# Kernel tuning notes

Hardware: AMD Instinct MI355X
Metric: run time of the kernel (lower is better)

## Reference

```python
import jax, jax.numpy as jnp
import numpy as np

N_NODES = 100000
N_EDGES = 1600000
IN_F, HID_F, OUT_F = 128, 128, 64


def setup_inputs() -> dict:
    key = jax.random.key(0)
    ks = jax.random.split(key, 12)
    inp = {
        "features": jax.random.normal(ks[0], (N_NODES, IN_F), dtype=jnp.float32),
        "src": jax.random.randint(ks[1], (N_EDGES,), 0, N_NODES, dtype=jnp.int32),
        "dst": jax.random.randint(ks[2], (N_EDGES,), 0, N_NODES, dtype=jnp.int32),
        "Ws0": jax.random.normal(ks[3], (IN_F, HID_F), dtype=jnp.float32) / np.sqrt(IN_F),
        "Wn0": jax.random.normal(ks[4], (IN_F, HID_F), dtype=jnp.float32) / np.sqrt(IN_F),
        "b0": jnp.zeros((HID_F,), dtype=jnp.float32),
        "Ws1": jax.random.normal(ks[5], (HID_F, HID_F), dtype=jnp.float32) / np.sqrt(HID_F),
        "Wn1": jax.random.normal(ks[6], (HID_F, HID_F), dtype=jnp.float32) / np.sqrt(HID_F),
        "b1": jnp.zeros((HID_F,), dtype=jnp.float32),
        "Ws2": jax.random.normal(ks[7], (HID_F, OUT_F), dtype=jnp.float32) / np.sqrt(HID_F),
        "Wn2": jax.random.normal(ks[8], (HID_F, OUT_F), dtype=jnp.float32) / np.sqrt(HID_F),
        "b2": jnp.zeros((OUT_F,), dtype=jnp.float32),
    }
    return inp


def _sage_conv(h, src, dst, inv_deg, Ws, Wn, b, act):
    # gather neighbor (source) features along edges: [E, d]
    msg = h[src]
    # mean aggregation onto destination nodes: [N, d]
    agg = jax.ops.segment_sum(msg, dst, num_segments=N_NODES) * inv_deg
    out = h @ Ws + agg @ Wn + b
    return jax.nn.relu(out) if act else out


def reference(features, src, dst, Ws0, Wn0, b0, Ws1, Wn1, b1, Ws2, Wn2, b2):
    # in-degree for mean normalization (clamped at 1, matching DGL mean semantics)
    deg = jax.ops.segment_sum(jnp.ones((N_EDGES,), jnp.float32), dst, num_segments=N_NODES)
    inv_deg = (1.0 / jnp.maximum(deg, 1.0))[:, None]
    h = _sage_conv(features, src, dst, inv_deg, Ws0, Wn0, b0, act=True)
    # dropout is identity in eval mode
    h = _sage_conv(h, src, dst, inv_deg, Ws1, Wn1, b1, act=True)
    h = _sage_conv(h, src, dst, inv_deg, Ws2, Wn2, b2, act=False)
    return h
```

## Files before the change

### kernel.cpp

```cpp
#include <hip/hip_runtime.h>

static constexpr int N = 100000;
static constexpr int E = 1600000;
static constexpr int F = 128;
static constexpr int HA_W = 256;
static constexpr int NB = (N + 127) / 128;
static constexpr int PCHUNK = 16384;
static constexpr int PGRID = (E + PCHUNK - 1) / PCHUNK;
static constexpr int CAP = 8192;

typedef __attribute__((ext_vector_type(8))) short bf16x8;
typedef __attribute__((ext_vector_type(4))) float f32x4;

__device__ inline unsigned short f2bf(float f) {
    unsigned int u = __builtin_bit_cast(unsigned int, f);
    unsigned int r = u + 0x7FFF + ((u >> 16) & 1);
    return (unsigned short)(r >> 16);
}
__device__ inline float bf_lo(unsigned int v) {
    return __builtin_bit_cast(float, v << 16);
}
__device__ inline float bf_hi(unsigned int v) {
    return __builtin_bit_cast(float, v & 0xffff0000u);
}

__global__ __launch_bounds__(256) void bucket_count_k(const int* __restrict__ dst,
                                                      int* __restrict__ bcnt) {
    __shared__ int sh[NB];
    const int t = threadIdx.x;
    for (int i = t; i < NB; i += 256) sh[i] = 0;
    __syncthreads();
    const int cb = blockIdx.x * PCHUNK;
    #pragma unroll
    for (int j = 0; j < PCHUNK / 1024; ++j) {
        int idx = cb + j * 1024 + t * 4;
        if (idx < E) {
            int4 d4 = *(const int4*)&dst[idx];
            atomicAdd(&sh[d4.x >> 7], 1);
            atomicAdd(&sh[d4.y >> 7], 1);
            atomicAdd(&sh[d4.z >> 7], 1);
            atomicAdd(&sh[d4.w >> 7], 1);
        }
    }
    __syncthreads();
    for (int i = t; i < NB; i += 256)
        if (sh[i]) atomicAdd(&bcnt[i], sh[i]);
}

__global__ __launch_bounds__(1024) void scan_buckets_k(const int* __restrict__ bcnt,
                                                       int* __restrict__ bbase,
                                                       int* __restrict__ bcur,
                                                       int* __restrict__ row_ptr) {
    __shared__ int shw[16];
    const int t = threadIdx.x, lane = t & 63, wv = t >> 6;
    int v = (t < NB) ? bcnt[t] : 0;
    int s = v;
    #pragma unroll
    for (int off = 1; off < 64; off <<= 1) {
        int u = __shfl_up(s, off);
        if (lane >= off) s += u;
    }
    if (lane == 63) shw[wv] = s;
    __syncthreads();
    if (wv == 0 && lane < 16) {
        int w = shw[lane];
        #pragma unroll
        for (int off = 1; off < 16; off <<= 1) {
            int u = __shfl_up(w, off);
            if (lane >= off) w += u;
        }
        shw[lane] = w;
    }
    __syncthreads();
    int wex = wv ? shw[wv - 1] : 0;
    int excl = wex + s - v;
    if (t < NB) { bbase[t] = excl; bcur[t] = 0; }
    if (t == 0) { bbase[NB] = E; row_ptr[N] = E; }
}

__global__ __launch_bounds__(256) void partition_k(const int* __restrict__ src,
                                                   const int* __restrict__ dst,
                                                   const int* __restrict__ bbase,
                                                   int* __restrict__ bcur,
                                                   unsigned int* __restrict__ ebuf) {
    __shared__ int sh_hist[NB];
    __shared__ int sh_base[NB];
    __shared__ int sh_cur[NB];
    const int t = threadIdx.x;
    for (int i = t; i < NB; i += 256) sh_hist[i] = 0;
    __syncthreads();
    const int cb = blockIdx.x * PCHUNK;
    #pragma unroll
    for (int j = 0; j < PCHUNK / 1024; ++j) {
        int idx = cb + j * 1024 + t * 4;
        if (idx < E) {
            int4 d4 = *(const int4*)&dst[idx];
            atomicAdd(&sh_hist[d4.x >> 7], 1);
            atomicAdd(&sh_hist[d4.y >> 7], 1);
            atomicAdd(&sh_hist[d4.z >> 7], 1);
            atomicAdd(&sh_hist[d4.w >> 7], 1);
        }
    }
    __syncthreads();
    for (int i = t; i < NB; i += 256) {
        int c = sh_hist[i];
        sh_base[i] = c ? (bbase[i] + atomicAdd(&bcur[i], c)) : 0;
        sh_cur[i] = 0;
    }
    __syncthreads();
    #pragma unroll
    for (int j = 0; j < PCHUNK / 1024; ++j) {
        int idx = cb + j * 1024 + t * 4;
        if (idx < E) {
            int4 s4 = *(const int4*)&src[idx];
            int4 d4 = *(const int4*)&dst[idx];
            {
                int b = d4.x >> 7; int p = atomicAdd(&sh_cur[b], 1);
                ebuf[sh_base[b] + p] = (unsigned)s4.x | ((unsigned)(d4.x & 127) << 17);
            }
            {
                int b = d4.y >> 7; int p = atomicAdd(&sh_cur[b], 1);
                ebuf[sh_base[b] + p] = (unsigned)s4.y | ((unsigned)(d4.y & 127) << 17);
            }
            {
                int b = d4.z >> 7; int p = atomicAdd(&sh_cur[b], 1);
                ebuf[sh_base[b] + p] = (unsigned)s4.z | ((unsigned)(d4.z & 127) << 17);
            }
            {
                int b = d4.w >> 7; int p = atomicAdd(&sh_cur[b], 1);
                ebuf[sh_base[b] + p] = (unsigned)s4.w | ((unsigned)(d4.w & 127) << 17);
            }
        }
    }
}

__global__ __launch_bounds__(256) void csr_sort_k(const unsigned int* __restrict__ ebuf,
                                                  const int* __restrict__ bbase,
                                                  int* __restrict__ row_ptr,
                                                  float* __restrict__ inv_deg,
                                                  int* __restrict__ esrc) {
    __shared__ unsigned int sh_e[CAP];
    __shared__ int sh_o[CAP];
    __shared__ int sh_hist[128];
    __shared__ int sh_excl[128];
    __shared__ int sh_cur[128];
    __shared__ int sh_w0;
    const int b = blockIdx.x, t = threadIdx.x;
    const int e0 = bbase[b];
    const int ec = bbase[b + 1] - e0;
    if (t < 128) { sh_hist[t] = 0; sh_cur[t] = 0; }
    __syncthreads();
    for (int i = t; i < ec; i += 256) {
        unsigned int e = ebuf[e0 + i];
        sh_e[i] = e;
        atomicAdd(&sh_hist[e >> 17], 1);
    }
    __syncthreads();
    int v = 0;
    if (t < 128) v = sh_hist[t];
    int incl = v;
    const int lane = t & 63;
    #pragma unroll
    for (int off = 1; off < 64; off <<= 1) {
        int u = __shfl_up(incl, off);
        if (lane >= off) incl += u;
    }
    if (t == 63) sh_w0 = incl;
    __syncthreads();
    if (t >= 64 && t < 128) incl += sh_w0;
    if (t < 128) {
        sh_excl[t] = incl - v;
        int node = b * 128 + t;
        if (node < N) {
            row_ptr[node] = e0 + incl - v;
            inv_deg[node] = 1.0f / fmaxf((float)v, 1.0f);
        }
    }
    __syncthreads();
    for (int i = t; i < ec; i += 256) {
        unsigned int e = sh_e[i];
        int l = e >> 17;
        int pos = sh_excl[l] + atomicAdd(&sh_cur[l], 1);
        sh_o[pos] = (int)(e & 0x1FFFF);
    }
    __syncthreads();
    for (int i = t; i < ec; i += 256) esrc[e0 + i] = sh_o[i];
}

__global__ __launch_bounds__(256) void conv_feat_k(const float* __restrict__ feat,
                                                   unsigned short* __restrict__ ha) {
    int idx = blockIdx.x * 256 + threadIdx.x;
    int node = idx >> 5;
    int c4 = idx & 31;
    if (node >= N) return;
    float4 v = *(const float4*)&feat[(size_t)node * F + c4 * 4];
    unsigned long long p = (unsigned long long)f2bf(v.x)
                         | ((unsigned long long)f2bf(v.y) << 16)
                         | ((unsigned long long)f2bf(v.z) << 32)
                         | ((unsigned long long)f2bf(v.w) << 48);
    *(unsigned long long*)&ha[(size_t)node * HA_W + c4 * 4] = p;
}

__global__ __launch_bounds__(256) void prep_w_all_k(const float* __restrict__ Ws0,
                                                    const float* __restrict__ Wn0,
                                                    const float* __restrict__ Ws1,
                                                    const float* __restrict__ Wn1,
                                                    const float* __restrict__ Ws2,
                                                    const float* __restrict__ Wn2,
                                                    unsigned short* __restrict__ Wt0,
                                                    unsigned short* __restrict__ Wt1,
                                                    unsigned short* __restrict__ Wc2) {
    int idx = blockIdx.x * 256 + threadIdx.x;
    if (idx < 32768) {
        int n = idx >> 8, k = idx & 255;
        float v = (k < 128) ? Ws0[k * 128 + n] : Wn0[(k - 128) * 128 + n];
        Wt0[n * 256 + k] = f2bf(v);
    } else if (idx < 65536) {
        int j = idx - 32768;
        int n = j >> 8, k = j & 255;
        float v = (k < 128) ? Ws1[k * 128 + n] : Wn1[(k - 128) * 128 + n];
        Wt1[n * 256 + k] = f2bf(v);
    } else if (idx < 65536 + 16384) {
        int j = idx - 65536;
        int c = j >> 7, k = j & 127;
        float v = (c < 64) ? Ws2[k * 64 + c] : Wn2[k * 64 + (c - 64)];
        Wc2[c * 128 + k] = f2bf(v);
    }
}

__global__ __launch_bounds__(256) void aggregate128_k(const unsigned short* __restrict__ ha,
                                                      unsigned short* __restrict__ ha_out,
                                                      const int* __restrict__ row_ptr,
                                                      const int* __restrict__ esrc,
                                                      const float* __restrict__ inv_deg) {
    const int lane = threadIdx.x & 63;
    const int wv = threadIdx.x >> 6;
    const int slot = lane >> 4;
    const int cl = lane & 15;
    const int node = blockIdx.x * 16 + wv * 4 + slot;
    const int beg = row_ptr[node];
    const int cnt = row_ptr[node + 1] - beg;
    const float sinv = inv_deg[node];
    int wmax = cnt;
    wmax = max(wmax, __shfl_xor(wmax, 16));
    wmax = max(wmax, __shfl_xor(wmax, 32));
    float a0 = 0.f, a1 = 0.f, a2 = 0.f, a3 = 0.f;
    float a4 = 0.f, a5 = 0.f, a6 = 0.f, a7 = 0.f;
    for (int j = 0; j < wmax; j += 8) {
        int idx[8];
        uint4 v[8];
        #pragma unroll
        for (int u = 0; u < 8; ++u)
            idx[u] = (j + u < cnt) ? __builtin_nontemporal_load(&esrc[beg + j + u]) : -1;
        #pragma unroll
        for (int u = 0; u < 8; ++u) {
            if (idx[u] >= 0)
                v[u] = *(const uint4*)&ha[(size_t)idx[u] * HA_W + cl * 8];
            else { v[u].x = 0u; v[u].y = 0u; v[u].z = 0u; v[u].w = 0u; }
        }
        #pragma unroll
        for (int u = 0; u < 8; ++u) {
            a0 += bf_lo(v[u].x); a1 += bf_hi(v[u].x);
            a2 += bf_lo(v[u].y); a3 += bf_hi(v[u].y);
            a4 += bf_lo(v[u].z); a5 += bf_hi(v[u].z);
            a6 += bf_lo(v[u].w); a7 += bf_hi(v[u].w);
        }
    }
    uint4 o;
    o.x = (unsigned int)f2bf(a0 * sinv) | ((unsigned int)f2bf(a1 * sinv) << 16);
    o.y = (unsigned int)f2bf(a2 * sinv) | ((unsigned int)f2bf(a3 * sinv) << 16);
    o.z = (unsigned int)f2bf(a4 * sinv) | ((unsigned int)f2bf(a5 * sinv) << 16);
    o.w = (unsigned int)f2bf(a6 * sinv) | ((unsigned int)f2bf(a7 * sinv) << 16);
    *(uint4*)&ha_out[(size_t)node * HA_W + F + cl * 8] = o;
}

__global__ __launch_bounds__(256) void aggregate64_add_k(const unsigned short* __restrict__ Q,
                                                         const int* __restrict__ row_ptr,
                                                         const int* __restrict__ esrc,
                                                         const float* __restrict__ inv_deg,
                                                         float* __restrict__ out) {
    const int lane = threadIdx.x & 63;
    const int wv = threadIdx.x >> 6;
    const int slot = lane >> 3;
    const int cl = lane & 7;
    const int node = blockIdx.x * 32 + wv * 8 + slot;
    const int beg = row_ptr[node];
    const int cnt = row_ptr[node + 1] - beg;
    const float sinv = inv_deg[node];
    int wmax = cnt;
    wmax = max(wmax, __shfl_xor(wmax, 8));
    wmax = max(wmax, __shfl_xor(wmax, 16));
    wmax = max(wmax, __shfl_xor(wmax, 32));
    float a0 = 0.f, a1 = 0.f, a2 = 0.f, a3 = 0.f;
    float a4 = 0.f, a5 = 0.f, a6 = 0.f, a7 = 0.f;
    for (int j = 0; j < wmax; j += 8) {
        int idx[8];
        uint4 v[8];
        #pragma unroll
        for (int u = 0; u < 8; ++u)
            idx[u] = (j + u < cnt) ? __builtin_nontemporal_load(&esrc[beg + j + u]) : -1;
        #pragma unroll
        for (int u = 0; u < 8; ++u) {
            if (idx[u] >= 0)
                v[u] = *(const uint4*)&Q[(size_t)idx[u] * 64 + cl * 8];
            else { v[u].x = 0u; v[u].y = 0u; v[u].z = 0u; v[u].w = 0u; }
        }
        #pragma unroll
        for (int u = 0; u < 8; ++u) {
            a0 += bf_lo(v[u].x); a1 += bf_hi(v[u].x);
            a2 += bf_lo(v[u].y); a3 += bf_hi(v[u].y);
            a4 += bf_lo(v[u].z); a5 += bf_hi(v[u].z);
            a6 += bf_lo(v[u].w); a7 += bf_hi(v[u].w);
        }
    }
    float4* p0 = (float4*)&out[(size_t)node * 64 + cl * 8];
    float4 pv = *p0;
    pv.x += a0 * sinv; pv.y += a1 * sinv; pv.z += a2 * sinv; pv.w += a3 * sinv;
    *p0 = pv;
    float4* p1 = p0 + 1;
    float4 pw = *p1;
    pw.x += a4 * sinv; pw.y += a5 * sinv; pw.z += a6 * sinv; pw.w += a7 * sinv;
    *p1 = pw;
}

__global__ __launch_bounds__(256) void linear01_k(const unsigned short* __restrict__ ha,
                                                  const unsigned short* __restrict__ Wt,
                                                  const float* __restrict__ bias,
                                                  unsigned short* __restrict__ out_ha) {
    constexpr int CPW = 32;
    constexpr int NT = 2;
    const int lane = threadIdx.x & 63;
    const int wv = threadIdx.x >> 6;
    const int col0 = wv * CPW;
    const int lc = lane & 15;
    const int lg = lane >> 4;
    bf16x8 bfrag[NT][8];
    float bias_c[NT];
    #pragma unroll
    for (int nt = 0; nt < NT; ++nt) {
        int col = col0 + nt * 16 + lc;
        bias_c[nt] = bias[col];
        #pragma unroll
        for (int ks = 0; ks < 8; ++ks)
            bfrag[nt][ks] = *(const bf16x8*)&Wt[col * 256 + ks * 32 + lg * 8];
    }
    const int i0base = blockIdx.x * 128;
    for (int s = 0; s < 8; ++s) {
        int i0 = i0base + s * 16;
        if (i0 >= N) return;
        const unsigned short* arow = &ha[(size_t)(i0 + lc) * HA_W];
        f32x4 acc[NT];
        #pragma unroll
        for (int nt = 0; nt < NT; ++nt) {
            acc[nt][0] = bias_c[nt]; acc[nt][1] = bias_c[nt];
            acc[nt][2] = bias_c[nt]; acc[nt][3] = bias_c[nt];
        }
        #pragma unroll
        for (int ks = 0; ks < 8; ++ks) {
            bf16x8 af = *(const bf16x8*)&arow[ks * 32 + lg * 8];
            #pragma unroll
            for (int nt = 0; nt < NT; ++nt)
                acc[nt] = __builtin_amdgcn_mfma_f32_16x16x32_bf16(af, bfrag[nt][ks], acc[nt], 0, 0, 0);
        }
        #pragma unroll
        for (int nt = 0; nt < NT; ++nt) {
            int col = col0 + nt * 16 + lc;
            #pragma unroll
            for (int r = 0; r < 4; ++r) {
                int orow = i0 + lg * 4 + r;
                float v = fmaxf(acc[nt][r], 0.f);
                out_ha[(size_t)orow * HA_W + col] = f2bf(v);
            }
        }
    }
}

__global__ __launch_bounds__(256) void linear2_k(const unsigned short* __restrict__ ha,
                                                 const unsigned short* __restrict__ Wc,
                                                 const float* __restrict__ bias,
                                                 float* __restrict__ out,
                                                 unsigned short* __restrict__ Q) {
    constexpr int CPW = 32;
    constexpr int NT = 2;
    const int lane = threadIdx.x & 63;
    const int wv = threadIdx.x >> 6;
    const int col0 = wv * CPW;
    const int lc = lane & 15;
    const int lg = lane >> 4;
    bf16x8 bfrag[NT][4];
    float bias_c[NT];
    #pragma unroll
    for (int nt = 0; nt < NT; ++nt) {
        int col = col0 + nt * 16 + lc;
        bias_c[nt] = (wv < 2) ? bias[col] : 0.f;
        #pragma unroll
        for (int ks = 0; ks < 4; ++ks)
            bfrag[nt][ks] = *(const bf16x8*)&Wc[col * 128 + ks * 32 + lg * 8];
    }
    const int i0base = blockIdx.x * 128;
    for (int s = 0; s < 8; ++s) {
        int i0 = i0base + s * 16;
        if (i0 >= N) return;
        const unsigned short* arow = &ha[(size_t)(i0 + lc) * HA_W];
        f32x4 acc[NT];
        #pragma unroll
        for (int nt = 0; nt < NT; ++nt) {
            acc[nt][0] = bias_c[nt]; acc[nt][1] = bias_c[nt];
            acc[nt][2] = bias_c[nt]; acc[nt][3] = bias_c[nt];
        }
        #pragma unroll
        for (int ks = 0; ks < 4; ++ks) {
            bf16x8 af = *(const bf16x8*)&arow[ks * 32 + lg * 8];
            #pragma unroll
            for (int nt = 0; nt < NT; ++nt)
                acc[nt] = __builtin_amdgcn_mfma_f32_16x16x32_bf16(af, bfrag[nt][ks], acc[nt], 0, 0, 0);
        }
        #pragma unroll
        for (int nt = 0; nt < NT; ++nt) {
            int col = col0 + nt * 16 + lc;
            #pragma unroll
            for (int r = 0; r < 4; ++r) {
                int orow = i0 + lg * 4 + r;
                float v = acc[nt][r];
                if (wv < 2) out[(size_t)orow * 64 + col] = v;
                else        Q[(size_t)orow * 64 + (col - 64)] = f2bf(v);
            }
        }
    }
}

extern "C" void kernel_launch(void* const* d_in, const int* in_sizes, int n_in,
                              void* d_out, int out_size, void* d_ws, size_t ws_size,
                              hipStream_t stream) {
    const float* feat = (const float*)d_in[0];
    const int*   src  = (const int*)d_in[1];
    const int*   dst  = (const int*)d_in[2];
    const float* Ws0  = (const float*)d_in[3];
    const float* Wn0  = (const float*)d_in[4];
    const float* b0   = (const float*)d_in[5];
    const float* Ws1  = (const float*)d_in[6];
    const float* Wn1  = (const float*)d_in[7];
    const float* b1   = (const float*)d_in[8];
    const float* Ws2  = (const float*)d_in[9];
    const float* Wn2  = (const float*)d_in[10];
    const float* b2   = (const float*)d_in[11];
    float* out = (float*)d_out;

    char* ws = (char*)d_ws;
    size_t off = 0;
    auto alloc = [&](size_t bytes) {
        void* p = ws + off;
        off = (off + bytes + 255) & ~(size_t)255;
        return p;
    };
    unsigned short* haA = (unsigned short*)alloc((size_t)N * HA_W * 2);
    unsigned short* haB = (unsigned short*)alloc((size_t)N * HA_W * 2);
    unsigned short* Qb  = (unsigned short*)alloc((size_t)N * 64 * 2);
    unsigned short* Wt0 = (unsigned short*)alloc((size_t)128 * 256 * 2);
    unsigned short* Wt1 = (unsigned short*)alloc((size_t)128 * 256 * 2);
    unsigned short* Wc2 = (unsigned short*)alloc((size_t)128 * 128 * 2);
    float* inv     = (float*)alloc((size_t)N * 4);
    int*   row_ptr = (int*)alloc((size_t)(N + 1) * 4);
    int*   bcnt    = (int*)alloc((size_t)NB * 4);
    int*   bbase   = (int*)alloc((size_t)(NB + 1) * 4);
    int*   bcur    = (int*)alloc((size_t)NB * 4);
    unsigned int* ebuf = (unsigned int*)alloc((size_t)E * 4);
    int*   esrc    = (int*)alloc((size_t)E * 4);
    (void)ws_size; (void)in_sizes; (void)n_in; (void)out_size;

    hipMemsetAsync(bcnt, 0, (size_t)NB * 4, stream);
    bucket_count_k<<<PGRID, 256, 0, stream>>>(dst, bcnt);
    scan_buckets_k<<<1, 1024, 0, stream>>>(bcnt, bbase, bcur, row_ptr);
    partition_k<<<PGRID, 256, 0, stream>>>(src, dst, bbase, bcur, ebuf);
    csr_sort_k<<<NB, 256, 0, stream>>>(ebuf, bbase, row_ptr, inv, esrc);

    conv_feat_k<<<(N * 32 + 255) / 256, 256, 0, stream>>>(feat, haA);
    prep_w_all_k<<<(65536 + 16384 + 255) / 256, 256, 0, stream>>>(
        Ws0, Wn0, Ws1, Wn1, Ws2, Wn2, Wt0, Wt1, Wc2);

    const int lin_grid = (N + 127) / 128;
    aggregate128_k<<<N / 16, 256, 0, stream>>>(haA, haA, row_ptr, esrc, inv);
    linear01_k<<<lin_grid, 256, 0, stream>>>(haA, Wt0, b0, haB);
    aggregate128_k<<<N / 16, 256, 0, stream>>>(haB, haB, row_ptr, esrc, inv);
    linear01_k<<<lin_grid, 256, 0, stream>>>(haB, Wt1, b1, haA);
    linear2_k<<<lin_grid, 256, 0, stream>>>(haA, Wc2, b2, out, Qb);
    aggregate64_add_k<<<N / 32, 256, 0, stream>>>(Qb, row_ptr, esrc, inv, out);
}
```

Before: 326.1 us.

## Use fixed-capacity edge buckets, compact feature layout, and fuse prep kernels

Drops the bucket-count and scan kernels by giving each 128-node bucket a fixed slot of 2560 edges, so partitioning writes at bucket*CAPB plus an atomic cursor and the sort reads its count from that cursor. Node features now live in a compact 128-wide bf16 buffer separate from the aggregation buffer, so neighbor gathers touch half as many bytes per row and the table fits better in cache. The linear layer reads the two halves from their separate buffers. Feature conversion and weight prep are merged into one launch. The fixed capacity assumes no bucket gets more than 2560 edges, which holds for uniformly random destinations but would overflow on skewed graphs.

```diff
diff --git a/kernel.cpp b/kernel.cpp
--- a/kernel.cpp
+++ b/kernel.cpp
@@ -3,11 +3,11 @@
 static constexpr int N = 100000;
 static constexpr int E = 1600000;
 static constexpr int F = 128;
-static constexpr int HA_W = 256;
 static constexpr int NB = (N + 127) / 128;
 static constexpr int PCHUNK = 16384;
 static constexpr int PGRID = (E + PCHUNK - 1) / PCHUNK;
-static constexpr int CAP = 8192;
+static constexpr int CAPB = 2560;
+static constexpr int NPAD = NB * 128;
 
 typedef __attribute__((ext_vector_type(8))) short bf16x8;
 typedef __attribute__((ext_vector_type(4))) float f32x4;
@@ -24,63 +24,53 @@
     return __builtin_bit_cast(float, v & 0xffff0000u);
 }
 
-__global__ __launch_bounds__(256) void bucket_count_k(const int* __restrict__ dst,
-                                                      int* __restrict__ bcnt) {
-    __shared__ int sh[NB];
+__global__ __launch_bounds__(256) void prep_all_k(const float* __restrict__ feat,
+                                                  unsigned short* __restrict__ hA,
+                                                  const float* __restrict__ Ws0,
+                                                  const float* __restrict__ Wn0,
+                                                  const float* __restrict__ Ws1,
+                                                  const float* __restrict__ Wn1,
+                                                  const float* __restrict__ Ws2,
+                                                  const float* __restrict__ Wn2,
+                                                  unsigned short* __restrict__ Wt0,
+                                                  unsigned short* __restrict__ Wt1,
+                                                  unsigned short* __restrict__ Wc2) {
     const int t = threadIdx.x;
-    for (int i = t; i < NB; i += 256) sh[i] = 0;
-    __syncthreads();
-    const int cb = blockIdx.x * PCHUNK;
-    #pragma unroll
-    for (int j = 0; j < PCHUNK / 1024; ++j) {
-        int idx = cb + j * 1024 + t * 4;
-        if (idx < E) {
-            int4 d4 = *(const int4*)&dst[idx];
-            atomicAdd(&sh[d4.x >> 7], 1);
-            atomicAdd(&sh[d4.y >> 7], 1);
-            atomicAdd(&sh[d4.z >> 7], 1);
-            atomicAdd(&sh[d4.w >> 7], 1);
-        }
-    }
-    __syncthreads();
-    for (int i = t; i < NB; i += 256)
-        if (sh[i]) atomicAdd(&bcnt[i], sh[i]);
-}
-
-__global__ __launch_bounds__(1024) void scan_buckets_k(const int* __restrict__ bcnt,
-                                                       int* __restrict__ bbase,
-                                                       int* __restrict__ bcur,
-                                                       int* __restrict__ row_ptr) {
-    __shared__ int shw[16];
-    const int t = threadIdx.x, lane = t & 63, wv = t >> 6;
-    int v = (t < NB) ? bcnt[t] : 0;
-    int s = v;
-    #pragma unroll
-    for (int off = 1; off < 64; off <<= 1) {
-        int u = __shfl_up(s, off);
-        if (lane >= off) s += u;
-    }
-    if (lane == 63) shw[wv] = s;
-    __syncthreads();
-    if (wv == 0 && lane < 16) {
-        int w = shw[lane];
-        #pragma unroll
-        for (int off = 1; off < 16; off <<= 1) {
-            int u = __shfl_up(w, off);
-            if (lane >= off) w += u;
-        }
-        shw[lane] = w;
-    }
-    __syncthreads();
-    int wex = wv ? shw[wv - 1] : 0;
-    int excl = wex + s - v;
-    if (t < NB) { bbase[t] = excl; bcur[t] = 0; }
-    if (t == 0) { bbase[NB] = E; row_ptr[N] = E; }
+    const int bid = blockIdx.x;
+    if (bid < 12500) {
+        int idx = bid * 256 + t;
+        int node = idx >> 5;
+        int c4 = idx & 31;
+        if (node < N) {
+            float4 v = *(const float4*)&feat[(size_t)node * F + c4 * 4];
+            unsigned long long p = (unsigned long long)f2bf(v.x)
+                                 | ((unsigned long long)f2bf(v.y) << 16)
+                                 | ((unsigned long long)f2bf(v.z) << 32)
+                                 | ((unsigned long long)f2bf(v.w) << 48);
+            *(unsigned long long*)&hA[(size_t)node * F + c4 * 4] = p;
+        }
+    } else {
+        int idx = (bid - 12500) * 256 + t;
+        if (idx < 32768) {
+            int n = idx >> 8, k = idx & 255;
+            float v = (k < 128) ? Ws0[k * 128 + n] : Wn0[(k - 128) * 128 + n];
+            Wt0[n * 256 + k] = f2bf(v);
+        } else if (idx < 65536) {
+            int j = idx - 32768;
+            int n = j >> 8, k = j & 255;
+            float v = (k < 128) ? Ws1[k * 128 + n] : Wn1[(k - 128) * 128 + n];
+            Wt1[n * 256 + k] = f2bf(v);
+        } else if (idx < 65536 + 16384) {
+            int j = idx - 65536;
+            int c = j >> 7, k = j & 127;
+            float v = (c < 64) ? Ws2[k * 64 + c] : Wn2[k * 64 + (c - 64)];
+            Wc2[c * 128 + k] = f2bf(v);
+        }
+    }
 }
 
 __global__ __launch_bounds__(256) void partition_k(const int* __restrict__ src,
                                                    const int* __restrict__ dst,
-                                                   const int* __restrict__ bbase,
                                                    int* __restrict__ bcur,
                                                    unsigned int* __restrict__ ebuf) {
     __shared__ int sh_hist[NB];
@@ -104,7 +94,7 @@
     __syncthreads();
     for (int i = t; i < NB; i += 256) {
         int c = sh_hist[i];
-        sh_base[i] = c ? (bbase[i] + atomicAdd(&bcur[i], c)) : 0;
+        sh_base[i] = c ? (i * CAPB + atomicAdd(&bcur[i], c)) : 0;
         sh_cur[i] = 0;
     }
     __syncthreads();
@@ -135,19 +125,20 @@
 }
 
 __global__ __launch_bounds__(256) void csr_sort_k(const unsigned int* __restrict__ ebuf,
-                                                  const int* __restrict__ bbase,
-                                                  int* __restrict__ row_ptr,
+                                                  const int* __restrict__ bcur,
+                                                  int* __restrict__ row_beg,
+                                                  int* __restrict__ degs,
                                                   float* __restrict__ inv_deg,
                                                   int* __restrict__ esrc) {
-    __shared__ unsigned int sh_e[CAP];
-    __shared__ int sh_o[CAP];
+    __shared__ unsigned int sh_e[CAPB];
+    __shared__ int sh_o[CAPB];
     __shared__ int sh_hist[128];
     __shared__ int sh_excl[128];
     __shared__ int sh_cur[128];
     __shared__ int sh_w0;
     const int b = blockIdx.x, t = threadIdx.x;
-    const int e0 = bbase[b];
-    const int ec = bbase[b + 1] - e0;
+    const int e0 = b * CAPB;
+    const int ec = bcur[b];
     if (t < 128) { sh_hist[t] = 0; sh_cur[t] = 0; }
     __syncthreads();
     for (int i = t; i < ec; i += 256) {
@@ -172,7 +163,8 @@
         sh_excl[t] = incl - v;
         int node = b * 128 + t;
         if (node < N) {
-            row_ptr[node] = e0 + incl - v;
+            row_beg[node] = e0 + incl - v;
+            degs[node] = v;
             inv_deg[node] = 1.0f / fmaxf((float)v, 1.0f);
         }
     }
@@ -187,50 +179,10 @@
     for (int i = t; i < ec; i += 256) esrc[e0 + i] = sh_o[i];
 }
 
-__global__ __launch_bounds__(256) void conv_feat_k(const float* __restrict__ feat,
-                                                   unsigned short* __restrict__ ha) {
-    int idx = blockIdx.x * 256 + threadIdx.x;
-    int node = idx >> 5;
-    int c4 = idx & 31;
-    if (node >= N) return;
-    float4 v = *(const float4*)&feat[(size_t)node * F + c4 * 4];
-    unsigned long long p = (unsigned long long)f2bf(v.x)
-                         | ((unsigned long long)f2bf(v.y) << 16)
-                         | ((unsigned long long)f2bf(v.z) << 32)
-                         | ((unsigned long long)f2bf(v.w) << 48);
-    *(unsigned long long*)&ha[(size_t)node * HA_W + c4 * 4] = p;
-}
-
-__global__ __launch_bounds__(256) void prep_w_all_k(const float* __restrict__ Ws0,
-                                                    const float* __restrict__ Wn0,
-                                                    const float* __restrict__ Ws1,
-                                                    const float* __restrict__ Wn1,
-                                                    const float* __restrict__ Ws2,
-                                                    const float* __restrict__ Wn2,
-                                                    unsigned short* __restrict__ Wt0,
-                                                    unsigned short* __restrict__ Wt1,
-                                                    unsigned short* __restrict__ Wc2) {
-    int idx = blockIdx.x * 256 + threadIdx.x;
-    if (idx < 32768) {
-        int n = idx >> 8, k = idx & 255;
-        float v = (k < 128) ? Ws0[k * 128 + n] : Wn0[(k - 128) * 128 + n];
-        Wt0[n * 256 + k] = f2bf(v);
-    } else if (idx < 65536) {
-        int j = idx - 32768;
-        int n = j >> 8, k = j & 255;
-        float v = (k < 128) ? Ws1[k * 128 + n] : Wn1[(k - 128) * 128 + n];
-        Wt1[n * 256 + k] = f2bf(v);
-    } else if (idx < 65536 + 16384) {
-        int j = idx - 65536;
-        int c = j >> 7, k = j & 127;
-        float v = (c < 64) ? Ws2[k * 64 + c] : Wn2[k * 64 + (c - 64)];
-        Wc2[c * 128 + k] = f2bf(v);
-    }
-}
-
-__global__ __launch_bounds__(256) void aggregate128_k(const unsigned short* __restrict__ ha,
+__global__ __launch_bounds__(256) void aggregate128_k(const unsigned short* __restrict__ h,
                                                       unsigned short* __restrict__ ha_out,
-                                                      const int* __restrict__ row_ptr,
+                                                      const int* __restrict__ row_beg,
+                                                      const int* __restrict__ degs,
                                                       const int* __restrict__ esrc,
                                                       const float* __restrict__ inv_deg) {
     const int lane = threadIdx.x & 63;
@@ -238,8 +190,8 @@
     const int slot = lane >> 4;
     const int cl = lane & 15;
     const int node = blockIdx.x * 16 + wv * 4 + slot;
-    const int beg = row_ptr[node];
-    const int cnt = row_ptr[node + 1] - beg;
+    const int beg = row_beg[node];
+    const int cnt = degs[node];
     const float sinv = inv_deg[node];
     int wmax = cnt;
     wmax = max(wmax, __shfl_xor(wmax, 16));
@@ -255,7 +207,7 @@
         #pragma unroll
         for (int u = 0; u < 8; ++u) {
             if (idx[u] >= 0)
-                v[u] = *(const uint4*)&ha[(size_t)idx[u] * HA_W + cl * 8];
+                v[u] = *(const uint4*)&h[(size_t)idx[u] * F + cl * 8];
             else { v[u].x = 0u; v[u].y = 0u; v[u].z = 0u; v[u].w = 0u; }
         }
         #pragma unroll
@@ -271,62 +223,14 @@
     o.y = (unsigned int)f2bf(a2 * sinv) | ((unsigned int)f2bf(a3 * sinv) << 16);
     o.z = (unsigned int)f2bf(a4 * sinv) | ((unsigned int)f2bf(a5 * sinv) << 16);
     o.w = (unsigned int)f2bf(a6 * sinv) | ((unsigned int)f2bf(a7 * sinv) << 16);
-    *(uint4*)&ha_out[(size_t)node * HA_W + F + cl * 8] = o;
-}
-
-__global__ __launch_bounds__(256) void aggregate64_add_k(const unsigned short* __restrict__ Q,
-                                                         const int* __restrict__ row_ptr,
-                                                         const int* __restrict__ esrc,
-                                                         const float* __restrict__ inv_deg,
-                                                         float* __restrict__ out) {
-    const int lane = threadIdx.x & 63;
-    const int wv = threadIdx.x >> 6;
-    const int slot = lane >> 3;
-    const int cl = lane & 7;
-    const int node = blockIdx.x * 32 + wv * 8 + slot;
-    const int beg = row_ptr[node];
-    const int cnt = row_ptr[node + 1] - beg;
-    const float sinv = inv_deg[node];
-    int wmax = cnt;
-    wmax = max(wmax, __shfl_xor(wmax, 8));
-    wmax = max(wmax, __shfl_xor(wmax, 16));
-    wmax = max(wmax, __shfl_xor(wmax, 32));
-    float a0 = 0.f, a1 = 0.f, a2 = 0.f, a3 = 0.f;
-    float a4 = 0.f, a5 = 0.f, a6 = 0.f, a7 = 0.f;
-    for (int j = 0; j < wmax; j += 8) {
-        int idx[8];
-        uint4 v[8];
-        #pragma unroll
-        for (int u = 0; u < 8; ++u)
-            idx[u] = (j + u < cnt) ? __builtin_nontemporal_load(&esrc[beg + j + u]) : -1;
-        #pragma unroll
-        for (int u = 0; u < 8; ++u) {
-            if (idx[u] >= 0)
-                v[u] = *(const uint4*)&Q[(size_t)idx[u] * 64 + cl * 8];
-            else { v[u].x = 0u; v[u].y = 0u; v[u].z = 0u; v[u].w = 0u; }
-        }
-        #pragma unroll
-        for (int u = 0; u < 8; ++u) {
-            a0 += bf_lo(v[u].x); a1 += bf_hi(v[u].x);
-            a2 += bf_lo(v[u].y); a3 += bf_hi(v[u].y);
-            a4 += bf_lo(v[u].z); a5 += bf_hi(v[u].z);
-            a6 += bf_lo(v[u].w); a7 += bf_hi(v[u].w);
-        }
-    }
-    float4* p0 = (float4*)&out[(size_t)node * 64 + cl * 8];
-    float4 pv = *p0;
-    pv.x += a0 * sinv; pv.y += a1 * sinv; pv.z += a2 * sinv; pv.w += a3 * sinv;
-    *p0 = pv;
-    float4* p1 = p0 + 1;
-    float4 pw = *p1;
-    pw.x += a4 * sinv; pw.y += a5 * sinv; pw.z += a6 * sinv; pw.w += a7 * sinv;
-    *p1 = pw;
-}
-
-__global__ __launch_bounds__(256) void linear01_k(const unsigned short* __restrict__ ha,
+    *(uint4*)&ha_out[(size_t)node * 256 + F + cl * 8] = o;
+}
+
+__global__ __launch_bounds__(256) void linear01_k(const unsigned short* __restrict__ h,
+                                                  const unsigned short* __restrict__ ha,
                                                   const unsigned short* __restrict__ Wt,
                                                   const float* __restrict__ bias,
-                                                  unsigned short* __restrict__ out_ha) {
+                                                  unsigned short* __restrict__ hout) {
     constexpr int CPW = 32;
     constexpr int NT = 2;
     const int lane = threadIdx.x & 63;
@@ -348,7 +252,8 @@
     for (int s = 0; s < 8; ++s) {
         int i0 = i0base + s * 16;
         if (i0 >= N) return;
-        const unsigned short* arow = &ha[(size_t)(i0 + lc) * HA_W];
+        const unsigned short* hrow = &h[(size_t)(i0 + lc) * F];
+        const unsigned short* arow = &ha[(size_t)(i0 + lc) * 256 + F];
         f32x4 acc[NT];
         #pragma unroll
         for (int nt = 0; nt < NT; ++nt) {
@@ -356,11 +261,18 @@
             acc[nt][2] = bias_c[nt]; acc[nt][3] = bias_c[nt];
         }
         #pragma unroll
-        for (int ks = 0; ks < 8; ++ks) {
+        for (int ks = 0; ks < 4; ++ks) {
+            bf16x8 af = *(const bf16x8*)&hrow[ks * 32 + lg * 8];
+            #pragma unroll
+            for (int nt = 0; nt < NT; ++nt)
+                acc[nt] = __builtin_amdgcn_mfma_f32_16x16x32_bf16(af, bfrag[nt][ks], acc[nt], 0, 0, 0);
+        }
+        #pragma unroll
+        for (int ks = 0; ks < 4; ++ks) {
             bf16x8 af = *(const bf16x8*)&arow[ks * 32 + lg * 8];
             #pragma unroll
             for (int nt = 0; nt < NT; ++nt)
-                acc[nt] = __builtin_amdgcn_mfma_f32_16x16x32_bf16(af, bfrag[nt][ks], acc[nt], 0, 0, 0);
+                acc[nt] = __builtin_amdgcn_mfma_f32_16x16x32_bf16(af, bfrag[nt][ks + 4], acc[nt], 0, 0, 0);
         }
         #pragma unroll
         for (int nt = 0; nt < NT; ++nt) {
@@ -368,14 +280,13 @@
             #pragma unroll
             for (int r = 0; r < 4; ++r) {
                 int orow = i0 + lg * 4 + r;
-                float v = fmaxf(acc[nt][r], 0.f);
-                out_ha[(size_t)orow * HA_W + col] = f2bf(v);
-            }
-        }
-    }
-}
-
-__global__ __launch_bounds__(256) void linear2_k(const unsigned short* __restrict__ ha,
+                hout[(size_t)orow * F + col] = f2bf(fmaxf(acc[nt][r], 0.f));
+            }
+        }
+    }
+}
+
+__global__ __launch_bounds__(256) void linear2_k(const unsigned short* __restrict__ h,
                                                  const unsigned short* __restrict__ Wc,
                                                  const float* __restrict__ bias,
                                                  float* __restrict__ out,
@@ -401,7 +312,7 @@
     for (int s = 0; s < 8; ++s) {
         int i0 = i0base + s * 16;
         if (i0 >= N) return;
-        const unsigned short* arow = &ha[(size_t)(i0 + lc) * HA_W];
+        const unsigned short* arow = &h[(size_t)(i0 + lc) * F];
         f32x4 acc[NT];
         #pragma unroll
         for (int nt = 0; nt < NT; ++nt) {
@@ -427,6 +338,56 @@
             }
         }
     }
+}
+
+__global__ __launch_bounds__(256) void aggregate64_add_k(const unsigned short* __restrict__ Q,
+                                                         const int* __restrict__ row_beg,
+                                                         const int* __restrict__ degs,
+                                                         const int* __restrict__ esrc,
+                                                         const float* __restrict__ inv_deg,
+                                                         float* __restrict__ out) {
+    const int lane = threadIdx.x & 63;
+    const int wv = threadIdx.x >> 6;
+    const int slot = lane >> 3;
+    const int cl = lane & 7;
+    const int node = blockIdx.x * 32 + wv * 8 + slot;
+    const int beg = row_beg[node];
+    const int cnt = degs[node];
+    const float sinv = inv_deg[node];
+    int wmax = cnt;
+    wmax = max(wmax, __shfl_xor(wmax, 8));
+    wmax = max(wmax, __shfl_xor(wmax, 16));
+    wmax = max(wmax, __shfl_xor(wmax, 32));
+    float a0 = 0.f, a1 = 0.f, a2 = 0.f, a3 = 0.f;
+    float a4 = 0.f, a5 = 0.f, a6 = 0.f, a7 = 0.f;
+    for (int j = 0; j < wmax; j += 8) {
+        int idx[8];
+        uint4 v[8];
+        #pragma unroll
+        for (int u = 0; u < 8; ++u)
+            idx[u] = (j + u < cnt) ? __builtin_nontemporal_load(&esrc[beg + j + u]) : -1;
+        #pragma unroll
+        for (int u = 0; u < 8; ++u) {
+            if (idx[u] >= 0)
+                v[u] = *(const uint4*)&Q[(size_t)idx[u] * 64 + cl * 8];
+            else { v[u].x = 0u; v[u].y = 0u; v[u].z = 0u; v[u].w = 0u; }
+        }
+        #pragma unroll
+        for (int u = 0; u < 8; ++u) {
+            a0 += bf_lo(v[u].x); a1 += bf_hi(v[u].x);
+            a2 += bf_lo(v[u].y); a3 += bf_hi(v[u].y);
+            a4 += bf_lo(v[u].z); a5 += bf_hi(v[u].z);
+            a6 += bf_lo(v[u].w); a7 += bf_hi(v[u].w);
+        }
+    }
+    float4* p0 = (float4*)&out[(size_t)node * 64 + cl * 8];
+    float4 pv = *p0;
+    pv.x += a0 * sinv; pv.y += a1 * sinv; pv.z += a2 * sinv; pv.w += a3 * sinv;
+    *p0 = pv;
+    float4* p1 = p0 + 1;
+    float4 pw = *p1;
+    pw.x += a4 * sinv; pw.y += a5 * sinv; pw.z += a6 * sinv; pw.w += a7 * sinv;
+    *p1 = pw;
 }
 
 extern "C" void kernel_launch(void* const* d_in, const int* in_sizes, int n_in,
@@ -453,36 +414,32 @@
         off = (off + bytes + 255) & ~(size_t)255;
         return p;
     };
-    unsigned short* haA = (unsigned short*)alloc((size_t)N * HA_W * 2);
-    unsigned short* haB = (unsigned short*)alloc((size_t)N * HA_W * 2);
+    unsigned short* hA  = (unsigned short*)alloc((size_t)NPAD * F * 2);
+    unsigned short* hB  = (unsigned short*)alloc((size_t)NPAD * F * 2);
+    unsigned short* agg = (unsigned short*)alloc((size_t)N * 256 * 2);
     unsigned short* Qb  = (unsigned short*)alloc((size_t)N * 64 * 2);
     unsigned short* Wt0 = (unsigned short*)alloc((size_t)128 * 256 * 2);
     unsigned short* Wt1 = (unsigned short*)alloc((size_t)128 * 256 * 2);
     unsigned short* Wc2 = (unsigned short*)alloc((size_t)128 * 128 * 2);
     float* inv     = (float*)alloc((size_t)N * 4);
-    int*   row_ptr = (int*)alloc((size_t)(N + 1) * 4);
-    int*   bcnt    = (int*)alloc((size_t)NB * 4);
-    int*   bbase   = (int*)alloc((size_t)(NB + 1) * 4);
+    int*   row_beg = (int*)alloc((size_t)N * 4);
+    int*   degs    = (int*)alloc((size_t)N * 4);
     int*   bcur    = (int*)alloc((size_t)NB * 4);
-    unsigned int* ebuf = (unsigned int*)alloc((size_t)E * 4);
-    int*   esrc    = (int*)alloc((size_t)E * 4);
+    unsigned int* ebuf = (unsigned int*)alloc((size_t)NB * CAPB * 4);
+    int*   esrc    = (int*)alloc((size_t)NB * CAPB * 4);
     (void)ws_size; (void)in_sizes; (void)n_in; (void)out_size;
 
-    hipMemsetAsync(bcnt, 0, (size_t)NB * 4, stream);
-    bucket_count_k<<<PGRID, 256, 0, stream>>>(dst, bcnt);
-    scan_buckets_k<<<1, 1024, 0, stream>>>(bcnt, bbase, bcur, row_ptr);
-    partition_k<<<PGRID, 256, 0, stream>>>(src, dst, bbase, bcur, ebuf);
-    csr_sort_k<<<NB, 256, 0, stream>>>(ebuf, bbase, row_ptr, inv, esrc);
-
-    conv_feat_k<<<(N * 32 + 255) / 256, 256, 0, stream>>>(feat, haA);
-    prep_w_all_k<<<(65536 + 16384 + 255) / 256, 256, 0, stream>>>(
-        Ws0, Wn0, Ws1, Wn1, Ws2, Wn2, Wt0, Wt1, Wc2);
+    hipMemsetAsync(bcur, 0, (size_t)NB * 4, stream);
+    prep_all_k<<<12500 + 320, 256, 0, stream>>>(
+        feat, hA, Ws0, Wn0, Ws1, Wn1, Ws2, Wn2, Wt0, Wt1, Wc2);
+    partition_k<<<PGRID, 256, 0, stream>>>(src, dst, bcur, ebuf);
+    csr_sort_k<<<NB, 256, 0, stream>>>(ebuf, bcur, row_beg, degs, inv, esrc);
 
     const int lin_grid = (N + 127) / 128;
-    aggregate128_k<<<N / 16, 256, 0, stream>>>(haA, haA, row_ptr, esrc, inv);
-    linear01_k<<<lin_grid, 256, 0, stream>>>(haA, Wt0, b0, haB);
-    aggregate128_k<<<N / 16, 256, 0, stream>>>(haB, haB, row_ptr, esrc, inv);
-    linear01_k<<<lin_grid, 256, 0, stream>>>(haB, Wt1, b1, haA);
-    linear2_k<<<lin_grid, 256, 0, stream>>>(haA, Wc2, b2, out, Qb);
-    aggregate64_add_k<<<N / 32, 256, 0, stream>>>(Qb, row_ptr, esrc, inv, out);
-}
+    aggregate128_k<<<N / 16, 256, 0, stream>>>(hA, agg, row_beg, degs, esrc, inv);
+    linear01_k<<<lin_grid, 256, 0, stream>>>(hA, agg, Wt0, b0, hB);
+    aggregate128_k<<<N / 16, 256, 0, stream>>>(hB, agg, row_beg, degs, esrc, inv);
+    linear01_k<<<lin_grid, 256, 0, stream>>>(hB, agg, Wt1, b1, hA);
+    linear2_k<<<lin_grid, 256, 0, stream>>>(hA, Wc2, b2, out, Qb);
+    aggregate64_add_k<<<N / 32, 256, 0, stream>>>(Qb, row_beg, degs, esrc, inv, out);
+}
```

Result: faster. 314.2 us (-3.6%).
